# Kernel tuning notes

Measured on AMD Instinct MI355X. Metric: run time of the kernel, lower is better.

The kernel has to match this reference:

```python
import jax, jax.numpy as jnp
import numpy as np

BIG = 1e10  # sentinel distance used by the original code


def _index_points(points, idx):
    # points: [B,N,C], idx: [B,N,8] -> [B,N,8,C]
    return jax.vmap(lambda p, i: p[i])(points, idx)


def _pointsift_select(radius, xyz):
    """Octant-wise nearest neighbor within radius. xyz: [B,N,3] -> idx int32 [B,N,8]."""
    B, N, _ = xyz.shape
    judge = radius ** 2
    # diff[b,n,p] = xyz[b,p] - xyz[b,n]
    diff = xyz[:, None, :, :] - xyz[:, :, None, :]            # [B,N,N,3]
    dist = jnp.sum(diff * diff, axis=-1)                      # [B,N,N]
    # octant code: ((p - n) + 1) truncated to int, dotted with [4,2,1]
    octw = jnp.array([4, 2, 1], dtype=jnp.int32)
    code = jnp.sum((diff + 1.0).astype(jnp.int32) * octw, axis=-1)  # [B,N,N]
    diag = jnp.eye(N, dtype=bool)[None]                       # self entry -> judge_dist
    idx_per_oct = []
    for i in range(8):
        d = jnp.where((code == i) & (dist > 1e-10) & (dist < judge), dist, BIG)
        d = jnp.where(diag, judge, d)
        idx_per_oct.append(jnp.argmin(d, axis=-1))            # first-min, matches torch.min
    return jnp.stack(idx_per_oct, axis=-1).astype(jnp.int32)  # [B,N,8]


def setup_inputs() -> dict:
    key = jax.random.key(0)
    k1, k2 = jax.random.split(key)
    B, N, C = 2, 4096, 64
    xyz = jax.random.uniform(k1, (B, N, 3), dtype=jnp.float32)
    points = jax.random.normal(k2, (B, N, C), dtype=jnp.float32)
    return {"xyz": xyz, "points": points, "radius": 0.25}


def reference(xyz, points, radius):
    B, N, _ = xyz.shape
    idx = _pointsift_select(radius, xyz)                      # [B,N,8]
    grouped_xyz = _index_points(xyz, idx) - xyz[:, :, None, :]  # [B,N,8,3]
    grouped_feats = _index_points(points, idx)                # [B,N,8,C]
    grouped_points = jnp.concatenate([grouped_xyz, grouped_feats], axis=-1)  # use_xyz=True
    return grouped_xyz, grouped_points, idx
```

## Files before the change

### kernel.cpp

```cpp
#include <hip/hip_runtime.h>

#define BB 2
#define NN 4096
#define CC 64
#define QPB 8
#define TPQ 32
#define NT 256

#define OUT0_OFF 0
#define OUT1_OFF (BB * NN * 8 * 3)
#define OUT2_OFF (OUT1_OFF + BB * NN * 8 * 67)

#define WS_SORTED_BYTES (BB * NN * 16)

__global__ __launch_bounds__(1024) void build_grid(
    const float* __restrict__ xyz, float4* __restrict__ sorted,
    int* __restrict__ offsets)
{
    __shared__ int hist[64];
    __shared__ int offs[65];
    const int b = blockIdx.x;
    const int tid = threadIdx.x;
    if (tid < 64) hist[tid] = 0;
    __syncthreads();
    const float* src = xyz + (size_t)b * NN * 3;
    #pragma unroll
    for (int p = tid; p < NN; p += 1024) {
        float x = src[p * 3 + 0], y = src[p * 3 + 1], z = src[p * 3 + 2];
        int cell = (((int)(x * 4.0f)) << 4) | (((int)(y * 4.0f)) << 2)
                 | ((int)(z * 4.0f));
        atomicAdd(&hist[cell], 1);
    }
    __syncthreads();
    if (tid < 64) {
        int inc = hist[tid];
        #pragma unroll
        for (int d = 1; d < 64; d <<= 1) {
            int u = __shfl_up(inc, d, 64);
            if (tid >= d) inc += u;
        }
        offs[tid + 1] = inc;
        if (tid == 0) offs[0] = 0;
    }
    __syncthreads();
    if (tid < 65) offsets[b * 65 + tid] = offs[tid];
    if (tid < 64) hist[tid] = offs[tid];
    __syncthreads();
    float4* dst = sorted + (size_t)b * NN;
    #pragma unroll
    for (int p = tid; p < NN; p += 1024) {
        float x = src[p * 3 + 0], y = src[p * 3 + 1], z = src[p * 3 + 2];
        int cell = (((int)(x * 4.0f)) << 4) | (((int)(y * 4.0f)) << 2)
                 | ((int)(z * 4.0f));
        int pos = atomicAdd(&hist[cell], 1);
        dst[pos] = make_float4(x, y, z, __uint_as_float((unsigned)p));
    }
}

__global__ __launch_bounds__(NT, 4) void select_gather(
    const float4* __restrict__ sorted, const int* __restrict__ offsets,
    const float* __restrict__ xyz, const float* __restrict__ points,
    const float* __restrict__ radius_p, float* __restrict__ out)
{
    __shared__ int s_off[65];
    __shared__ int s_res[QPB * 8];

    const int tid = threadIdx.x;
    const int blk = blockIdx.x;
    const int b = blk >> 9;
    const int qslot = (blk & 511) * QPB;
    const float4* sb = sorted + (size_t)b * NN;

    if (tid < 65) s_off[tid] = offsets[b * 65 + tid];

    const float r = radius_p[0];
    const float judge = __fmul_rn(r, r);
    const unsigned OFFC = __float_as_uint(1e-10f) + 1u;
    const unsigned seedkey = __float_as_uint(judge) - OFFC;

    const int g = tid >> 5;
    const float4 q = sb[qslot + g];
    const unsigned n = __float_as_uint(q.w);
    const float qx = q.x, qy = q.y, qz = q.z;
    const int sub = tid & (TPQ - 1);

    unsigned long long bv[8];
    const unsigned long long seed64 = ((unsigned long long)seedkey << 32) | n;
    #pragma unroll
    for (int o = 0; o < 8; ++o) bv[o] = seed64;

    float mnx = 1e9f, mxx = -1e9f, mny = 1e9f, mxy = -1e9f, mnz = 1e9f, mxz = -1e9f;
    #pragma unroll
    for (int k = 0; k < QPB; ++k) {
        float4 qq = sb[qslot + k];
        mnx = fminf(mnx, qq.x); mxx = fmaxf(mxx, qq.x);
        mny = fminf(mny, qq.y); mxy = fmaxf(mxy, qq.y);
        mnz = fminf(mnz, qq.z); mxz = fmaxf(mxz, qq.z);
    }
    const int lx = max(0, (int)((mnx - r) * 4.0f));
    const int hx = min(3, (int)((mxx + r) * 4.0f));
    const int ly = max(0, (int)((mny - r) * 4.0f));
    const int hy = min(3, (int)((mxy + r) * 4.0f));
    const int lz = max(0, (int)((mnz - r) * 4.0f));
    const int hz = min(3, (int)((mxz + r) * 4.0f));

    __syncthreads();

    for (int cx = lx; cx <= hx; ++cx) {
        for (int cy = ly; cy <= hy; ++cy) {
            const int cb = (cx << 4) | (cy << 2);
            const int s = s_off[cb + lz];
            const int e = s_off[cb + hz + 1];
            #pragma unroll 2
            for (int p = s + sub; p < e; p += TPQ) {
                float4 c = sb[p];
                float dx = __fsub_rn(c.x, qx);
                float dy = __fsub_rn(c.y, qy);
                float dz = __fsub_rn(c.z, qz);
                float dist = __fadd_rn(__fadd_rn(__fmul_rn(dx, dx),
                                                 __fmul_rn(dy, dy)),
                                       __fmul_rn(dz, dz));
                unsigned ikey = __float_as_uint(dist) - OFFC;
                ikey = (dist >= judge) ? 0xFFFFFFFFu : ikey;
                int code = (((int)__fadd_rn(dx, 1.0f)) * 4 +
                            ((int)__fadd_rn(dy, 1.0f)) * 2 +
                            ((int)__fadd_rn(dz, 1.0f)));
                unsigned long long key64 =
                    ((unsigned long long)ikey << 32) |
                    (unsigned long long)__float_as_uint(c.w);
                #pragma unroll
                for (int o = 0; o < 8; ++o) {
                    unsigned long long cand =
                        (code == o) ? key64 : 0xFFFFFFFFFFFFFFFFull;
                    bv[o] = (cand < bv[o]) ? cand : bv[o];
                }
            }
        }
    }

    #pragma unroll
    for (int mm = 1; mm < TPQ; mm <<= 1) {
        #pragma unroll
        for (int o = 0; o < 8; ++o) {
            unsigned long long ov = __shfl_xor(bv[o], mm, 64);
            if (ov < bv[o]) bv[o] = ov;
        }
    }

    if (sub == 0) {
        const size_t tb = ((size_t)b * NN + n) * 8;
        #pragma unroll
        for (int o = 0; o < 8; ++o) {
            int w = (int)(unsigned)(bv[o] & 0xFFFFFFFFu);
            s_res[g * 8 + o] = w;
            out[OUT2_OFF + tb + o] = (float)w;
        }
    }
    __syncthreads();

    const float* xb = xyz + (size_t)b * NN * 3;
    const float* pb = points + (size_t)b * NN * CC;
    #pragma unroll
    for (int o = 0; o < 8; ++o) {
        const int i = s_res[g * 8 + o];
        const size_t t = ((size_t)b * NN + n) * 8 + o;
        {
            const int c = sub;
            float v;
            if (c < 3) {
                v = __fsub_rn(xb[i * 3 + c], xb[n * 3 + c]);
                out[OUT0_OFF + t * 3 + c] = v;
            } else {
                v = pb[(size_t)i * CC + (c - 3)];
            }
            out[OUT1_OFF + t * 67 + c] = v;
        }
        {
            const int c = sub + 32;
            out[OUT1_OFF + t * 67 + c] = pb[(size_t)i * CC + (c - 3)];
        }
        if (sub < 3) {
            const int c = sub + 64;
            out[OUT1_OFF + t * 67 + c] = pb[(size_t)i * CC + (c - 3)];
        }
    }
}

extern "C" void kernel_launch(void* const* d_in, const int* in_sizes, int n_in,
                              void* d_out, int out_size, void* d_ws, size_t ws_size,
                              hipStream_t stream) {
    const float* xyz    = (const float*)d_in[0];
    const float* points = (const float*)d_in[1];
    const float* radius = (const float*)d_in[2];
    float* out = (float*)d_out;
    float4* ws_sorted = (float4*)d_ws;
    int* ws_offsets = (int*)((char*)d_ws + WS_SORTED_BYTES);

    hipLaunchKernelGGL(build_grid, dim3(BB), dim3(1024), 0, stream,
                       xyz, ws_sorted, ws_offsets);
    hipLaunchKernelGGL(select_gather,
                       dim3(BB * (NN / QPB)), dim3(NT), 0, stream,
                       ws_sorted, ws_offsets, xyz, points, radius, out);
}
```

Measured before the change: 112.5 us.

## Split select and gather into separate kernels with per-query cell bounds

```diff
diff --git a/kernel.cpp b/kernel.cpp
--- a/kernel.cpp
+++ b/kernel.cpp
@@ -3,8 +3,8 @@
 #define BB 2
 #define NN 4096
 #define CC 64
-#define QPB 8
-#define TPQ 32
+#define QPB 4
+#define TPQ 64
 #define NT 256
 
 #define OUT0_OFF 0
@@ -57,18 +57,16 @@
     }
 }
 
-__global__ __launch_bounds__(NT, 4) void select_gather(
+__global__ __launch_bounds__(NT, 8) void pointsift_select(
     const float4* __restrict__ sorted, const int* __restrict__ offsets,
-    const float* __restrict__ xyz, const float* __restrict__ points,
     const float* __restrict__ radius_p, float* __restrict__ out)
 {
     __shared__ int s_off[65];
-    __shared__ int s_res[QPB * 8];
 
     const int tid = threadIdx.x;
     const int blk = blockIdx.x;
-    const int b = blk >> 9;
-    const int qslot = (blk & 511) * QPB;
+    const int b = blk >> 10;
+    const int qslot = (blk & 1023) * QPB;
     const float4* sb = sorted + (size_t)b * NN;
 
     if (tid < 65) s_off[tid] = offsets[b * 65 + tid];
@@ -78,31 +76,23 @@
     const unsigned OFFC = __float_as_uint(1e-10f) + 1u;
     const unsigned seedkey = __float_as_uint(judge) - OFFC;
 
-    const int g = tid >> 5;
+    const int g = tid >> 6;
     const float4 q = sb[qslot + g];
     const unsigned n = __float_as_uint(q.w);
     const float qx = q.x, qy = q.y, qz = q.z;
-    const int sub = tid & (TPQ - 1);
+    const int sub = tid & 63;
 
     unsigned long long bv[8];
     const unsigned long long seed64 = ((unsigned long long)seedkey << 32) | n;
     #pragma unroll
     for (int o = 0; o < 8; ++o) bv[o] = seed64;
 
-    float mnx = 1e9f, mxx = -1e9f, mny = 1e9f, mxy = -1e9f, mnz = 1e9f, mxz = -1e9f;
-    #pragma unroll
-    for (int k = 0; k < QPB; ++k) {
-        float4 qq = sb[qslot + k];
-        mnx = fminf(mnx, qq.x); mxx = fmaxf(mxx, qq.x);
-        mny = fminf(mny, qq.y); mxy = fmaxf(mxy, qq.y);
-        mnz = fminf(mnz, qq.z); mxz = fmaxf(mxz, qq.z);
-    }
-    const int lx = max(0, (int)((mnx - r) * 4.0f));
-    const int hx = min(3, (int)((mxx + r) * 4.0f));
-    const int ly = max(0, (int)((mny - r) * 4.0f));
-    const int hy = min(3, (int)((mxy + r) * 4.0f));
-    const int lz = max(0, (int)((mnz - r) * 4.0f));
-    const int hz = min(3, (int)((mxz + r) * 4.0f));
+    const int lx = max(0, (int)((qx - r) * 4.0f));
+    const int hx = min(3, (int)((qx + r) * 4.0f));
+    const int ly = max(0, (int)((qy - r) * 4.0f));
+    const int hy = min(3, (int)((qy + r) * 4.0f));
+    const int lz = max(0, (int)((qz - r) * 4.0f));
+    const int hz = min(3, (int)((qz + r) * 4.0f));
 
     __syncthreads();
 
@@ -150,39 +140,43 @@
     if (sub == 0) {
         const size_t tb = ((size_t)b * NN + n) * 8;
         #pragma unroll
-        for (int o = 0; o < 8; ++o) {
-            int w = (int)(unsigned)(bv[o] & 0xFFFFFFFFu);
-            s_res[g * 8 + o] = w;
-            out[OUT2_OFF + tb + o] = (float)w;
-        }
-    }
-    __syncthreads();
-
-    const float* xb = xyz + (size_t)b * NN * 3;
-    const float* pb = points + (size_t)b * NN * CC;
-    #pragma unroll
-    for (int o = 0; o < 8; ++o) {
-        const int i = s_res[g * 8 + o];
-        const size_t t = ((size_t)b * NN + n) * 8 + o;
-        {
-            const int c = sub;
-            float v;
-            if (c < 3) {
-                v = __fsub_rn(xb[i * 3 + c], xb[n * 3 + c]);
-                out[OUT0_OFF + t * 3 + c] = v;
-            } else {
-                v = pb[(size_t)i * CC + (c - 3)];
-            }
-            out[OUT1_OFF + t * 67 + c] = v;
-        }
-        {
-            const int c = sub + 32;
-            out[OUT1_OFF + t * 67 + c] = pb[(size_t)i * CC + (c - 3)];
-        }
-        if (sub < 3) {
-            const int c = sub + 64;
-            out[OUT1_OFF + t * 67 + c] = pb[(size_t)i * CC + (c - 3)];
-        }
+        for (int o = 0; o < 8; ++o)
+            out[OUT2_OFF + tb + o] = (float)(unsigned)(bv[o] & 0xFFFFFFFFu);
+    }
+}
+
+#define GT_TPW 8
+__global__ __launch_bounds__(256, 8) void pointsift_gather(
+    const float* __restrict__ xyz, const float* __restrict__ points,
+    float* __restrict__ out)
+{
+    const int tid = threadIdx.x;
+    const int wave = tid >> 6;
+    const int lane = tid & 63;
+    const int base_t = (blockIdx.x * 4 + wave) * GT_TPW;
+
+    int idxs[GT_TPW];
+    #pragma unroll
+    for (int k = 0; k < GT_TPW; ++k)
+        idxs[k] = (int)out[OUT2_OFF + base_t + k];
+
+    #pragma unroll
+    for (int k = 0; k < GT_TPW; ++k) {
+        const int t = base_t + k;
+        const int i = idxs[k];
+        const int bn = t >> 3;
+        const int b = bn >> 12;
+        const int n = bn & (NN - 1);
+        const float* xb = xyz + (size_t)b * NN * 3;
+        const float* pb = points + (size_t)b * NN * CC;
+        float v;
+        if (lane < 3) v = __fsub_rn(xb[i * 3 + lane], xb[n * 3 + lane]);
+        else          v = pb[(size_t)i * CC + (lane - 3)];
+        out[OUT1_OFF + (size_t)t * 67 + lane] = v;
+        if (lane >= 61)
+            out[OUT1_OFF + (size_t)t * 67 + (lane + 3)] = pb[(size_t)i * CC + lane];
+        if (lane < 3)
+            out[OUT0_OFF + (size_t)t * 3 + lane] = v;
     }
 }
 
@@ -198,7 +192,10 @@
 
     hipLaunchKernelGGL(build_grid, dim3(BB), dim3(1024), 0, stream,
                        xyz, ws_sorted, ws_offsets);
-    hipLaunchKernelGGL(select_gather,
+    hipLaunchKernelGGL(pointsift_select,
                        dim3(BB * (NN / QPB)), dim3(NT), 0, stream,
-                       ws_sorted, ws_offsets, xyz, points, radius, out);
-}
+                       ws_sorted, ws_offsets, radius, out);
+    hipLaunchKernelGGL(pointsift_gather,
+                       dim3(BB * NN * 8 / (4 * GT_TPW)), dim3(256), 0, stream,
+                       xyz, points, out);
+}
```

Result: faster. 103.2 us (-8.3%).
